# Kernel optimization log

Hardware: AMD Instinct MI355X
Metric: run time of the kernel (lower is better)

Reference implementation:

```python
import jax, jax.numpy as jnp
import numpy as np

B, T, D = 32, 512, 240
HF, PF = 1024, 512
HB, PB = 1024, 512
BWD_BLOCK = 32
CLIP = 1.0


def setup_inputs() -> dict:
    key = jax.random.key(0)
    ks = jax.random.split(key, 8)
    u = lambda k, shape: jax.random.uniform(k, shape, jnp.float32, -0.05, 0.05)
    return {
        "data": jax.random.normal(ks[0], (B, T, D), jnp.float32),
        "mask": jnp.ones((B, T), jnp.float32),
        "weight_x_fwd": u(ks[1], (4 * HF, D)),
        "weight_r_fwd": u(ks[2], (4 * HF, PF)),
        "weight_bias_fwd": jnp.zeros((1, 4 * HF), jnp.float32),
        "weight_p_fwd": u(ks[3], (PF, HF)),
        "weight_x_bwd": u(ks[4], (4 * HB, D)),
        "weight_r_bwd": u(ks[5], (4 * HB, PB)),
        "weight_bias_bwd": jnp.zeros((1, 4 * HB), jnp.float32),
        "weight_p_bwd": u(ks[6], (PB, HB)),
    }


def _lstmp_scan(xg, wr, wp, mask, clip, hidden):
    """LSTM-with-projection scan.
    xg:   [T, N, 4H] precomputed input-side gate pre-activations (incl. bias)
    wr:   [4H, P] recurrent weights acting on projected state
    wp:   [P, H] projection weights
    mask: [T, N, 1] float mask (state held where mask==0)
    """
    N = xg.shape[1]
    P = wp.shape[0]
    c0 = jnp.zeros((N, hidden), xg.dtype)
    r0 = jnp.zeros((N, P), xg.dtype)

    def step(carry, inp):
        c, r = carry
        gx, m = inp
        gates = gx + r @ wr.T                      # [N, 4H]
        i, f, g, o = jnp.split(gates, 4, axis=-1)
        i = jax.nn.sigmoid(i)
        f = jax.nn.sigmoid(f)
        g = jnp.tanh(g)
        o = jax.nn.sigmoid(o)
        c_new = jnp.clip(f * c + i * g, -clip, clip)  # cell clipping
        r_new = (o * jnp.tanh(c_new)) @ wp.T          # project H -> P
        c = m * c_new + (1.0 - m) * c
        r = m * r_new + (1.0 - m) * r
        return (c, r), r

    _, rs = jax.lax.scan(step, (c0, r0), (xg, mask))
    return rs  # [T, N, P]


def reference(data, mask, weight_x_fwd, weight_r_fwd, weight_bias_fwd, weight_p_fwd,
              weight_x_bwd, weight_r_bwd, weight_bias_bwd, weight_p_bwd):
    Bx, Tx, _ = data.shape
    m = mask[..., None]  # [B, T, 1]

    # ---- forward direction: full left-to-right scan ----
    xg_f = jnp.einsum('btd,gd->tbg', data, weight_x_fwd) + weight_bias_fwd[0]
    m_f = jnp.swapaxes(m, 0, 1)  # [T, B, 1]
    out_f = _lstmp_scan(xg_f, weight_r_fwd, weight_p_fwd, m_f, CLIP, HF)
    out_f = jnp.swapaxes(out_f, 0, 1)  # [B, T, PF]

    # ---- backward direction: right-to-left within blocks of BWD_BLOCK ----
    L = BWD_BLOCK
    nb = Tx // L
    xg_b = jnp.einsum('btd,gd->btg', data, weight_x_bwd) + weight_bias_bwd[0]
    # split into blocks and reverse time within each block; blocks become batch
    xg_b = xg_b.reshape(Bx, nb, L, 4 * HB)[:, :, ::-1]
    xg_b = xg_b.transpose(2, 0, 1, 3).reshape(L, Bx * nb, 4 * HB)
    m_b = m.reshape(Bx, nb, L, 1)[:, :, ::-1].transpose(2, 0, 1, 3).reshape(L, Bx * nb, 1)
    out_b = _lstmp_scan(xg_b, weight_r_bwd, weight_p_bwd, m_b, CLIP, HB)
    out_b = out_b.reshape(L, Bx, nb, PB).transpose(1, 2, 0, 3)[:, :, ::-1]
    out_b = out_b.reshape(Bx, Tx, PB)

    return jnp.concatenate([out_f, out_b], axis=-1)  # [B, T, PF+PB]
```

## Files before the change

kernel.cpp:

```cpp
#include <hip/hip_runtime.h>
#include <hip/hip_bf16.h>
#include <math.h>


typedef __bf16 bf16_t;
typedef __bf16 bf16x8 __attribute__((ext_vector_type(8)));
typedef float f32x4 __attribute__((ext_vector_type(4)));
typedef unsigned int uint32;
typedef unsigned long long u64;

#define DEV __device__ __forceinline__

DEV bf16x8 ldg8(const bf16_t* p) { return *reinterpret_cast<const bf16x8*>(p); }
DEV bf16x8 ld_llc8(const bf16_t* p) {
  union { bf16x8 v; u64 q[2]; } u;
  u64* pp = (u64*)p;
  u.q[0] = __hip_atomic_load(pp, __ATOMIC_RELAXED, __HIP_MEMORY_SCOPE_AGENT);
  u.q[1] = __hip_atomic_load(pp + 1, __ATOMIC_RELAXED, __HIP_MEMORY_SCOPE_AGENT);
  return u.v;
}
DEV void st_llc_u32(uint32* p, uint32 v) {
  __hip_atomic_store(p, v, __ATOMIC_RELAXED, __HIP_MEMORY_SCOPE_AGENT);
}
DEV f32x4 mfma16(bf16x8 a, bf16x8 b, f32x4 c) {
  return __builtin_amdgcn_mfma_f32_16x16x32_bf16(a, b, c, 0, 0, 0);
}
DEV float sigmoidf_(float x) { return 1.0f / (1.0f + __expf(-x)); }
DEV float tanhf_(float x) {
  float e = __expf(2.0f * x);
  return (e - 1.0f) / (e + 1.0f);
}
DEV unsigned short bfbits(float x) {
  union { __bf16 b; unsigned short s; } u; u.b = (bf16_t)x; return u.s;
}

struct Params {
  const float* data;
  const float* mask;
  const float* wx_f; const float* wr_f; const float* bias_f; const float* wp_f;
  const float* wx_b; const float* wr_b; const float* bias_b; const float* wp_b;
  float* out;
  bf16_t* data_bf;
  bf16_t* Wf;
  bf16_t* Wb;
  bf16_t* wrf;
  bf16_t* wpT;
  bf16_t* wpf;
  bf16_t* wpb;
  float* bias_f_p;
  float* bias_b_p;
  bf16_t* h_hist;
  bf16_t* h_buf;
  bf16_t* r_buf;
  f32x4*  chb;
  int* fcnt;
  int* bcA;
  int* bcC;
};

DEV void poll_ge(int* p, int tgt) {
  while (__hip_atomic_load(p, __ATOMIC_RELAXED, __HIP_MEMORY_SCOPE_AGENT) < tgt)
    __builtin_amdgcn_s_sleep(1);
}
DEV void st_slot(int* p, int v) {
  __hip_atomic_store(p, v, __ATOMIC_RELAXED, __HIP_MEMORY_SCOPE_AGENT);
}
DEV void drain_sync() {
  asm volatile("s_waitcnt vmcnt(0)" ::: "memory");
  __syncthreads();
}

__global__ void k_data(Params P) {
  int idx = blockIdx.x * 256 + threadIdx.x;
  int k = idx & 255; int row = idx >> 8;
  float v = (k < 240) ? P.data[(size_t)row * 240 + k] : 0.0f;
  P.data_bf[idx] = (bf16_t)v;
}

__global__ void k_prep_w(Params P) {
  int idx = blockIdx.x * 256 + threadIdx.x;
  int n = 4096 * 512;
  if (idx < n) { P.wrf[idx] = (bf16_t)P.wr_f[idx]; return; }
  idx -= n; n = 1024 * 512;
  if (idx < n) { int h = idx >> 9, p = idx & 511;
                 P.wpT[idx] = (bf16_t)P.wp_f[(size_t)p * 1024 + h]; return; }
  idx -= n; n = 512 * 1024;
  if (idx < n) { P.wpf[idx] = (bf16_t)P.wp_f[idx]; return; }
  idx -= n; n = 512 * 1024;
  if (idx < n) { P.wpb[idx] = (bf16_t)P.wp_b[idx]; return; }
}

__global__ void k_packf(Params P) {
  int pr = blockIdx.x, k = threadIdx.x;
  int jj = pr >> 5, lr = pr & 31, grp = lr >> 3, uu = lr & 7;
  int grow = grp * 1024 + jj * 8 + uu;
  float v = (k < 240) ? P.wx_f[(size_t)grow * 240 + k] : 0.0f;
  P.Wf[(size_t)pr * 1280 + 1024 + k] = (bf16_t)v;
  if (k == 0) P.bias_f_p[pr] = P.bias_f[grow];
}

__global__ void k_packb(Params P) {
  int pr = blockIdx.x; int k = blockIdx.y * 256 + threadIdx.x;
  int ut = pr >> 8, rem = pr & 255, grp = rem >> 6, uu = rem & 63;
  int grow = grp * 1024 + ut * 64 + uu;
  float v;
  if (k < 512) v = P.wr_b[(size_t)grow * 512 + k];
  else { int kx = k - 512; v = (kx < 240) ? P.wx_b[(size_t)grow * 240 + kx] : 0.0f; }
  P.Wb[(size_t)pr * 768 + k] = (bf16_t)v;
  if (k == 0) P.bias_b_p[pr] = P.bias_b[grow];
}

__global__ void wc_gemm(Params P) {
  int tid = threadIdx.x, lane = tid & 63, wave = tid >> 6;
  int lane15 = lane & 15, laneh = lane >> 4;
  int mt = blockIdx.x >> 4, nt = blockIdx.x & 15;
  f32x4 acc[4] = {};
  for (int kc = 0; kc < 16; ++kc) {
    int kl = kc * 32 + laneh * 8;
    bf16x8 bv = ldg8(P.wpT + (size_t)(nt * 64 + wave * 16 + lane15) * 512 + kl);
#pragma unroll
    for (int mh = 0; mh < 4; ++mh) {
      bf16x8 av = ldg8(P.wrf + (size_t)(mt * 64 + mh * 16 + lane15) * 512 + kl);
      acc[mh] = mfma16(av, bv, acc[mh]);
    }
  }
#pragma unroll
  for (int mh = 0; mh < 4; ++mh)
#pragma unroll
    for (int q = 0; q < 4; ++q) {
      int m = mt * 64 + mh * 16 + laneh * 4 + q;
      int grp = m >> 10, unit = m & 1023, jj = unit >> 3, u8 = unit & 7;
      int pr = jj * 32 + grp * 8 + u8;
      int ncol = nt * 64 + wave * 16 + lane15;
      P.Wf[(size_t)pr * 1280 + ncol] = (bf16_t)acc[mh][q];
    }
}

__global__ void __launch_bounds__(256, 1) scan_kernel(Params P) {
  __shared__ union SM {
    float red[4][2][2][16][17];
    float gates[4][64][64];
  } sm;
  const int tid = threadIdx.x;
  const int lane = tid & 63, wave = tid >> 6;
  const int lane15 = lane & 15, laneh = lane >> 4;

  if (blockIdx.x < 128) {
    const int j = blockIdx.x;
    const bf16_t* Wfp = P.Wf + (size_t)(j * 32) * 1280;
    bf16x8 wh[2][8], wx[2][2];
#pragma unroll
    for (int nh = 0; nh < 2; ++nh) {
#pragma unroll
      for (int kc = 0; kc < 8; ++kc)
        wh[nh][kc] = ldg8(Wfp + (size_t)(nh * 16 + lane15) * 1280 +
                          wave * 256 + kc * 32 + laneh * 8);
#pragma unroll
      for (int kc = 0; kc < 2; ++kc)
        wx[nh][kc] = ldg8(Wfp + (size_t)(nh * 16 + lane15) * 1280 +
                          1024 + wave * 64 + kc * 32 + laneh * 8);
    }
    const int cb = tid >> 2, up = tid & 3;
    float biasr[2][4];
    if (tid < 128) {
#pragma unroll
      for (int e = 0; e < 2; ++e)
#pragma unroll
        for (int g = 0; g < 4; ++g)
          biasr[e][g] = P.bias_f_p[j * 32 + g * 8 + 2 * up + e];
    }
    float c_st[2] = {0.f, 0.f}, h_st[2] = {0.f, 0.f};

    for (int t = 0; t < 512; ++t) {
      float mk = 0.0f;
      if (tid < 128) mk = P.mask[cb * 512 + t];
      f32x4 acc[2][2] = {};
      {
        bf16x8 ax[2][2];
#pragma unroll
        for (int kc = 0; kc < 2; ++kc) {
          int kx = wave * 64 + kc * 32 + laneh * 8;
          ax[0][kc] = ldg8(P.data_bf + ((size_t)(lane15 * 512 + t)) * 256 + kx);
          ax[1][kc] = ldg8(P.data_bf + ((size_t)((16 + lane15) * 512 + t)) * 256 + kx);
        }
#pragma unroll
        for (int kc = 0; kc < 2; ++kc)
#pragma unroll
          for (int m = 0; m < 2; ++m) {
            acc[m][0] = mfma16(ax[m][kc], wx[0][kc], acc[m][0]);
            acc[m][1] = mfma16(ax[m][kc], wx[1][kc], acc[m][1]);
          }
      }
      if (t > 0) {
        poll_ge(P.fcnt + tid * 16, t);
        asm volatile("" ::: "memory");
        const bf16_t* hrow = P.h_hist + (size_t)(t - 1) * 32768;
        bf16x8 ah[2][8];
#pragma unroll
        for (int kc = 0; kc < 8; ++kc) {
          int kl = wave * 256 + kc * 32 + laneh * 8;
          ah[0][kc] = ldg8(hrow + (size_t)lane15 * 1024 + kl);
          ah[1][kc] = ldg8(hrow + (size_t)(16 + lane15) * 1024 + kl);
        }
#pragma unroll
        for (int kc = 0; kc < 8; ++kc)
#pragma unroll
          for (int m = 0; m < 2; ++m) {
            acc[m][0] = mfma16(ah[m][kc], wh[0][kc], acc[m][0]);
            acc[m][1] = mfma16(ah[m][kc], wh[1][kc], acc[m][1]);
          }
      }
      __syncthreads();
#pragma unroll
      for (int m = 0; m < 2; ++m)
#pragma unroll
        for (int nh = 0; nh < 2; ++nh)
#pragma unroll
          for (int q = 0; q < 4; ++q)
            sm.red[wave][m][nh][laneh * 4 + q][lane15] = acc[m][nh][q];
      __syncthreads();

      if (tid < 128) {
        uint32 pk = 0;
#pragma unroll
        for (int e = 0; e < 2; ++e) {
          float g4[4];
#pragma unroll
          for (int g = 0; g < 4; ++g) {
            int lr = g * 8 + 2 * up + e;
            float v = biasr[e][g];
#pragma unroll
            for (int w2 = 0; w2 < 4; ++w2)
              v += sm.red[w2][cb >> 4][lr >> 4][cb & 15][lr & 15];
            g4[g] = v;
          }
          float iv = sigmoidf_(g4[0]);
          float fv = sigmoidf_(g4[1]);
          float gv = tanhf_(g4[2]);
          float ov = sigmoidf_(g4[3]);
          float cnew = fminf(1.0f, fmaxf(-1.0f, fv * c_st[e] + iv * gv));
          float hnew = ov * tanhf_(cnew);
          c_st[e] = mk * cnew + (1.0f - mk) * c_st[e];
          h_st[e] = mk * hnew + (1.0f - mk) * h_st[e];
          pk |= ((uint32)bfbits(h_st[e])) << (16 * e);
        }
        st_llc_u32((uint32*)(P.h_hist + (size_t)t * 32768 + cb * 1024 + j * 8 + 2 * up), pk);
      }
      if (wave < 2) {
        asm volatile("s_waitcnt vmcnt(0)" ::: "memory");
        if (lane == 0) st_slot(&P.fcnt[(j * 2 + wave) * 16], t + 1);
      }
    }
  } else {
    const int bx = blockIdx.x - 128;
    const int btA = bx >> 4, utA = bx & 15;
    const int btC = bx >> 3, ptC = bx & 7;
    const int un = tid & 31, nr = tid >> 5;
    float biasB[2][4];
#pragma unroll
    for (int e = 0; e < 2; ++e)
#pragma unroll
      for (int g = 0; g < 4; ++g)
        biasB[e][g] = P.bias_b_p[utA * 256 + g * 64 + 2 * un + e];

    for (int s = 0; s < 32; ++s) {
      if (s > 0) {
        if (tid < 16) {
          int bxp = (btA * 2 + (tid >> 3)) * 8 + (tid & 7);
          poll_ge(P.bcC + bxp * 16, s);
        }
        __syncthreads();
        asm volatile("" ::: "memory");
      } else {
        __syncthreads();
      }
      f32x4 acc[4][4] = {};
      const bf16_t* WbBase = P.Wb + (size_t)(utA * 256 + wave * 64) * 768;
      for (int kc = 0; kc < 24; ++kc) {
        int kb = kc * 32;
        if (kb < 512 && s == 0) continue;
        int kl = kb + laneh * 8;
        bf16x8 av[4];
        if (kb < 512) {
#pragma unroll
          for (int mh = 0; mh < 4; ++mh)
            av[mh] = ld_llc8(P.r_buf + (size_t)(btA * 64 + mh * 16 + lane15) * 512 + kl);
        } else {
          int kx = kl - 512;
#pragma unroll
          for (int mh = 0; mh < 4; ++mh) {
            int n = btA * 64 + mh * 16 + lane15;
            int t2 = (n & 15) * 32 + 31 - s;
            av[mh] = ldg8(P.data_bf + ((size_t)((n >> 4) * 512 + t2)) * 256 + kx);
          }
        }
#pragma unroll
        for (int nf = 0; nf < 4; ++nf) {
          bf16x8 bv = ldg8(WbBase + (size_t)(nf * 16 + lane15) * 768 + kl);
#pragma unroll
          for (int mh = 0; mh < 4; ++mh)
            acc[mh][nf] = mfma16(av[mh], bv, acc[mh][nf]);
        }
      }
#pragma unroll
      for (int mh = 0; mh < 4; ++mh)
#pragma unroll
        for (int nf = 0; nf < 4; ++nf)
#pragma unroll
          for (int q = 0; q < 4; ++q)
            sm.gates[wave][mh * 16 + laneh * 4 + q][nf * 16 + lane15] = acc[mh][nf][q];
      __syncthreads();

      for (int ii = 0; ii < 8; ++ii) {
        int n = ii * 8 + nr;
        int ng = btA * 64 + n;
        int b = ng >> 4;
        int t2 = (ng & 15) * 32 + 31 - s;
        float mk = P.mask[b * 512 + t2];
        size_t cix = (size_t)ng * 512 + utA * 32 + un;
        f32x4 chv;
        if (s == 0) { chv[0] = 0.f; chv[1] = 0.f; chv[2] = 0.f; chv[3] = 0.f; }
        else chv = P.chb[cix];
        uint32 pk = 0;
#pragma unroll
        for (int e = 0; e < 2; ++e) {
          float gi = sm.gates[0][n][2 * un + e] + biasB[e][0];
          float gf = sm.gates[1][n][2 * un + e] + biasB[e][1];
          float gg = sm.gates[2][n][2 * un + e] + biasB[e][2];
          float go = sm.gates[3][n][2 * un + e] + biasB[e][3];
          float iv = sigmoidf_(gi), fv = sigmoidf_(gf);
          float gv = tanhf_(gg), ov = sigmoidf_(go);
          float cold = chv[2 * e], hold = chv[2 * e + 1];
          float cnew = fminf(1.0f, fmaxf(-1.0f, fv * cold + iv * gv));
          float hnew = ov * tanhf_(cnew);
          float cm = mk * cnew + (1.0f - mk) * cold;
          float hm = mk * hnew + (1.0f - mk) * hold;
          chv[2 * e] = cm; chv[2 * e + 1] = hm;
          pk |= ((uint32)bfbits(hm)) << (16 * e);
        }
        P.chb[cix] = chv;
        st_llc_u32((uint32*)(P.h_buf + (size_t)ng * 1024 + utA * 64 + 2 * un), pk);
      }
      drain_sync();
      if (tid == 0) st_slot(&P.bcA[bx * 16], s + 1);

      if (tid < 16) poll_ge(P.bcA + ((btC >> 1) * 16 + tid) * 16, s + 1);
      __syncthreads();
      asm volatile("" ::: "memory");
      f32x4 acc2[2] = {};
      for (int kc = 0; kc < 32; ++kc) {
        int kl = kc * 32 + laneh * 8;
        bf16x8 bv = ldg8(P.wpb + (size_t)(ptC * 64 + wave * 16 + lane15) * 1024 + kl);
        bf16x8 a0 = ld_llc8(P.h_buf + (size_t)(btC * 32 + lane15) * 1024 + kl);
        bf16x8 a1 = ld_llc8(P.h_buf + (size_t)(btC * 32 + 16 + lane15) * 1024 + kl);
        acc2[0] = mfma16(a0, bv, acc2[0]);
        acc2[1] = mfma16(a1, bv, acc2[1]);
      }
#pragma unroll
      for (int mh = 0; mh < 2; ++mh)
#pragma unroll
        for (int q = 0; q < 4; ++q) {
          int nl = mh * 16 + laneh * 4 + q;
          int ng = btC * 32 + nl;
          int b = ng >> 4;
          int t2 = (ng & 15) * 32 + 31 - s;
          int p = ptC * 64 + wave * 16 + lane15;
          float v = acc2[mh][q];
          P.out[((size_t)b * 512 + t2) * 1024 + 512 + p] = v;
          float v2 = __shfl_xor(v, 1);
          if (!(lane & 1)) {
            uint32 pk = ((uint32)bfbits(v2) << 16) | bfbits(v);
            st_llc_u32((uint32*)(P.r_buf + (size_t)ng * 512 + p), pk);
          }
        }
      drain_sync();
      if (tid == 0) st_slot(&P.bcC[bx * 16], s + 1);
    }
  }
}

__global__ void fwd_proj(Params P) {
  int tid = threadIdx.x, lane = tid & 63, wave = tid >> 6;
  int lane15 = lane & 15, laneh = lane >> 4;
  int mt = blockIdx.x >> 3, nt = blockIdx.x & 7;
  f32x4 acc[4] = {};
  for (int kc = 0; kc < 32; ++kc) {
    int kl = kc * 32 + laneh * 8;
    bf16x8 bv = ldg8(P.wpf + (size_t)(nt * 64 + wave * 16 + lane15) * 1024 + kl);
#pragma unroll
    for (int mh = 0; mh < 4; ++mh) {
      bf16x8 av = ldg8(P.h_hist + (size_t)(mt * 64 + mh * 16 + lane15) * 1024 + kl);
      acc[mh] = mfma16(av, bv, acc[mh]);
    }
  }
#pragma unroll
  for (int mh = 0; mh < 4; ++mh)
#pragma unroll
    for (int q = 0; q < 4; ++q) {
      int m = mt * 64 + mh * 16 + laneh * 4 + q;
      int t = m >> 5, nb = m & 31;
      int p = nt * 64 + wave * 16 + lane15;
      P.out[((size_t)nb * 512 + t) * 1024 + p] = acc[mh][q];
    }
}

extern "C" void kernel_launch(void* const* d_in, const int* in_sizes, int n_in,
                              void* d_out, int out_size, void* d_ws, size_t ws_size,
                              hipStream_t stream) {
  (void)in_sizes; (void)n_in; (void)out_size; (void)ws_size;
  Params P;
  P.data   = (const float*)d_in[0];
  P.mask   = (const float*)d_in[1];
  P.wx_f   = (const float*)d_in[2];
  P.wr_f   = (const float*)d_in[3];
  P.bias_f = (const float*)d_in[4];
  P.wp_f   = (const float*)d_in[5];
  P.wx_b   = (const float*)d_in[6];
  P.wr_b   = (const float*)d_in[7];
  P.bias_b = (const float*)d_in[8];
  P.wp_b   = (const float*)d_in[9];
  P.out    = (float*)d_out;

  char* ws = (char*)d_ws;
  size_t o = 0;
  auto take = [&](size_t bytes) -> char* {
    char* p = ws + o; o += (bytes + 255) & ~(size_t)255; return p;
  };
  P.data_bf  = (bf16_t*)take(32ull * 512 * 256 * 2);
  P.Wf       = (bf16_t*)take(4096ull * 1280 * 2);
  P.Wb       = (bf16_t*)take(4096ull * 768 * 2);
  P.wrf      = (bf16_t*)take(4096ull * 512 * 2);
  P.wpT      = (bf16_t*)take(1024ull * 512 * 2);
  P.wpf      = (bf16_t*)take(512ull * 1024 * 2);
  P.wpb      = (bf16_t*)take(512ull * 1024 * 2);
  P.bias_f_p = (float*)take(4096 * 4);
  P.bias_b_p = (float*)take(4096 * 4);
  P.h_hist   = (bf16_t*)take(512ull * 32 * 1024 * 2);
  P.h_buf    = (bf16_t*)take(512ull * 1024 * 2);
  P.r_buf    = (bf16_t*)take(512ull * 512 * 2);
  P.chb      = (f32x4*)take(512ull * 512 * 16);
  size_t fcnt_i = 256ull * 16, bc_i = 128ull * 16;
  char* cnts = take((fcnt_i + 2 * bc_i) * 4);
  P.fcnt = (int*)cnts;
  P.bcA  = (int*)(cnts + fcnt_i * 4);
  P.bcC  = (int*)(cnts + (fcnt_i + bc_i) * 4);

  hipMemsetAsync(cnts, 0, (fcnt_i + 2 * bc_i) * 4, stream);
  k_data<<<16384, 256, 0, stream>>>(P);
  k_prep_w<<<14336, 256, 0, stream>>>(P);
  k_packf<<<4096, 256, 0, stream>>>(P);
  k_packb<<<dim3(4096, 3), 256, 0, stream>>>(P);
  wc_gemm<<<1024, 256, 0, stream>>>(P);
  scan_kernel<<<256, 256, 0, stream>>>(P);
  fwd_proj<<<2048, 256, 0, stream>>>(P);
}
```

Baseline: 2.594 ms.

## Fuse forward projection GEMM into scan kernel, overlapping with backward blocks

Removes the separate fwd_proj launch and has the backward-direction blocks compute the forward projection tiles once the matching forward timesteps are published, polling the forward counters with a slower sleep. This is meant to hide the projection GEMM under the sequential forward scan and save a launch. It also moves the x-side MFMAs after the poll so the data loads can be issued early. Dynamic shared padding is added, likely to force one block per CU. The cost is that backward blocks now poll and compete for memory bandwidth with the critical-path forward recurrence.

```diff
diff --git a/kernel.cpp b/kernel.cpp
--- a/kernel.cpp
+++ b/kernel.cpp
@@ -62,6 +62,10 @@
   while (__hip_atomic_load(p, __ATOMIC_RELAXED, __HIP_MEMORY_SCOPE_AGENT) < tgt)
     __builtin_amdgcn_s_sleep(1);
 }
+DEV void poll_ge_slow(int* p, int tgt) {
+  while (__hip_atomic_load(p, __ATOMIC_RELAXED, __HIP_MEMORY_SCOPE_AGENT) < tgt)
+    __builtin_amdgcn_s_sleep(16);
+}
 DEV void st_slot(int* p, int v) {
   __hip_atomic_store(p, v, __ATOMIC_RELAXED, __HIP_MEMORY_SCOPE_AGENT);
 }
@@ -137,6 +141,8 @@
 }
 
 __global__ void __launch_bounds__(256, 1) scan_kernel(Params P) {
+  extern __shared__ char dyn_pad_[];
+  (void)dyn_pad_;
   __shared__ union SM {
     float red[4][2][2][16][17];
     float gates[4][64][64];
@@ -174,23 +180,14 @@
     for (int t = 0; t < 512; ++t) {
       float mk = 0.0f;
       if (tid < 128) mk = P.mask[cb * 512 + t];
+      bf16x8 ax0[2], ax1[2];
+#pragma unroll
+      for (int kc = 0; kc < 2; ++kc) {
+        int kx = wave * 64 + kc * 32 + laneh * 8;
+        ax0[kc] = ldg8(P.data_bf + ((size_t)(lane15 * 512 + t)) * 256 + kx);
+        ax1[kc] = ldg8(P.data_bf + ((size_t)((16 + lane15) * 512 + t)) * 256 + kx);
+      }
       f32x4 acc[2][2] = {};
-      {
-        bf16x8 ax[2][2];
-#pragma unroll
-        for (int kc = 0; kc < 2; ++kc) {
-          int kx = wave * 64 + kc * 32 + laneh * 8;
-          ax[0][kc] = ldg8(P.data_bf + ((size_t)(lane15 * 512 + t)) * 256 + kx);
-          ax[1][kc] = ldg8(P.data_bf + ((size_t)((16 + lane15) * 512 + t)) * 256 + kx);
-        }
-#pragma unroll
-        for (int kc = 0; kc < 2; ++kc)
-#pragma unroll
-          for (int m = 0; m < 2; ++m) {
-            acc[m][0] = mfma16(ax[m][kc], wx[0][kc], acc[m][0]);
-            acc[m][1] = mfma16(ax[m][kc], wx[1][kc], acc[m][1]);
-          }
-      }
       if (t > 0) {
         poll_ge(P.fcnt + tid * 16, t);
         asm volatile("" ::: "memory");
@@ -203,12 +200,27 @@
           ah[1][kc] = ldg8(hrow + (size_t)(16 + lane15) * 1024 + kl);
         }
 #pragma unroll
+        for (int kc = 0; kc < 2; ++kc) {
+          acc[0][0] = mfma16(ax0[kc], wx[0][kc], acc[0][0]);
+          acc[0][1] = mfma16(ax0[kc], wx[1][kc], acc[0][1]);
+          acc[1][0] = mfma16(ax1[kc], wx[0][kc], acc[1][0]);
+          acc[1][1] = mfma16(ax1[kc], wx[1][kc], acc[1][1]);
+        }
+#pragma unroll
         for (int kc = 0; kc < 8; ++kc)
 #pragma unroll
           for (int m = 0; m < 2; ++m) {
             acc[m][0] = mfma16(ah[m][kc], wh[0][kc], acc[m][0]);
             acc[m][1] = mfma16(ah[m][kc], wh[1][kc], acc[m][1]);
           }
+      } else {
+#pragma unroll
+        for (int kc = 0; kc < 2; ++kc) {
+          acc[0][0] = mfma16(ax0[kc], wx[0][kc], acc[0][0]);
+          acc[0][1] = mfma16(ax0[kc], wx[1][kc], acc[0][1]);
+          acc[1][0] = mfma16(ax1[kc], wx[0][kc], acc[1][0]);
+          acc[1][1] = mfma16(ax1[kc], wx[1][kc], acc[1][1]);
+        }
       }
       __syncthreads();
 #pragma unroll
@@ -376,32 +388,34 @@
       drain_sync();
       if (tid == 0) st_slot(&P.bcC[bx * 16], s + 1);
     }
+
+    for (int tile = bx; tile < 2048; tile += 128) {
+      int mt = tile >> 3, nt = tile & 7;
+      poll_ge_slow(P.fcnt + tid * 16, 2 * mt + 2);
+      __syncthreads();
+      asm volatile("" ::: "memory");
+      f32x4 acc[4] = {};
+      for (int kc = 0; kc < 32; ++kc) {
+        int kl = kc * 32 + laneh * 8;
+        bf16x8 bv = ldg8(P.wpf + (size_t)(nt * 64 + wave * 16 + lane15) * 1024 + kl);
+#pragma unroll
+        for (int mh = 0; mh < 4; ++mh) {
+          bf16x8 av = ldg8(P.h_hist + (size_t)(mt * 64 + mh * 16 + lane15) * 1024 + kl);
+          acc[mh] = mfma16(av, bv, acc[mh]);
+        }
+      }
+#pragma unroll
+      for (int mh = 0; mh < 4; ++mh)
+#pragma unroll
+        for (int q = 0; q < 4; ++q) {
+          int m = mt * 64 + mh * 16 + laneh * 4 + q;
+          int t = m >> 5, nb = m & 31;
+          int p = nt * 64 + wave * 16 + lane15;
+          P.out[((size_t)nb * 512 + t) * 1024 + p] = acc[mh][q];
+        }
+      __syncthreads();
+    }
   }
-}
-
-__global__ void fwd_proj(Params P) {
-  int tid = threadIdx.x, lane = tid & 63, wave = tid >> 6;
-  int lane15 = lane & 15, laneh = lane >> 4;
-  int mt = blockIdx.x >> 3, nt = blockIdx.x & 7;
-  f32x4 acc[4] = {};
-  for (int kc = 0; kc < 32; ++kc) {
-    int kl = kc * 32 + laneh * 8;
-    bf16x8 bv = ldg8(P.wpf + (size_t)(nt * 64 + wave * 16 + lane15) * 1024 + kl);
-#pragma unroll
-    for (int mh = 0; mh < 4; ++mh) {
-      bf16x8 av = ldg8(P.h_hist + (size_t)(mt * 64 + mh * 16 + lane15) * 1024 + kl);
-      acc[mh] = mfma16(av, bv, acc[mh]);
-    }
-  }
-#pragma unroll
-  for (int mh = 0; mh < 4; ++mh)
-#pragma unroll
-    for (int q = 0; q < 4; ++q) {
-      int m = mt * 64 + mh * 16 + laneh * 4 + q;
-      int t = m >> 5, nb = m & 31;
-      int p = nt * 64 + wave * 16 + lane15;
-      P.out[((size_t)nb * 512 + t) * 1024 + p] = acc[mh][q];
-    }
 }
 
 extern "C" void kernel_launch(void* const* d_in, const int* in_sizes, int n_in,
@@ -451,6 +465,5 @@
   k_packf<<<4096, 256, 0, stream>>>(P);
   k_packb<<<dim3(4096, 3), 256, 0, stream>>>(P);
   wc_gemm<<<1024, 256, 0, stream>>>(P);
-  scan_kernel<<<256, 256, 0, stream>>>(P);
-  fwd_proj<<<2048, 256, 0, stream>>>(P);
-}
+  scan_kernel<<<256, 256, 36864, stream>>>(P);
+}
```

Result: faster. 2.436 ms (-6.1%).
